# Performance work log

Hardware: AMD Instinct MI355X
Metric: run time of the kernel (lower is better)

Reference implementation:

```python
import jax, jax.numpy as jnp
import numpy as np

U, D, N, R = 256, 5120, 16, 160  # num_users, d_inner, d_state, dt_rank


def setup_inputs() -> dict:
    key = jax.random.key(0)
    ks = jax.random.split(key, 7)
    s = 0.02
    return {
        "x": jax.random.normal(ks[0], (U, D), jnp.float32),
        "delta_t_proj_w": jax.random.normal(ks[1], (D, R), jnp.float32) * s,
        "dt_proj_w": jax.random.normal(ks[2], (R, D), jnp.float32) * s,
        "dt_proj_b": jax.random.normal(ks[3], (D,), jnp.float32) * s,
        "B_proj_w": jax.random.normal(ks[4], (D, N), jnp.float32) * s,
        "abar": jax.random.uniform(ks[5], (U, D, N), jnp.float32),
        "hidden_state": jax.random.normal(ks[6], (U, D, N), jnp.float32),
    }


def reference(x, delta_t_proj_w, dt_proj_w, dt_proj_b, B_proj_w, abar, hidden_state):
    # delta: [U, D] -- low-rank dt projection then softplus
    dt = jax.nn.softplus(x @ delta_t_proj_w @ dt_proj_w + dt_proj_b)
    # B: [U, N]
    B = x @ B_proj_w
    # bbar[u,i,n] = dt[u,i] * B[u,n]  (discretized B, broadcast over d_inner x d_state)
    bbar = dt[:, :, None] * B[:, None, :]
    # h_new = abar * h + bbar * x   (selective-scan single step)
    h_new = abar * hidden_state + bbar * x[:, :, None]
    return h_new
```

## Files before the change

### kernel.cpp

```cpp
#include <hip/hip_runtime.h>
#include <math.h>

#define U_ 256
#define D_ 5120
#define N_ 16
#define R_ 160
#define J_ 176
#define KB 16

typedef float f4v __attribute__((ext_vector_type(4)));

__device__ __forceinline__ float softplus_f(float v) {
    return v > 20.f ? v : log1pf(__expf(v));
}

template<int NKS_T>
__global__ __launch_bounds__(256) void proj_partial(
    const float* __restrict__ x, const float* __restrict__ w1,
    const float* __restrict__ bw, float* __restrict__ P)
{
    constexpr int KSLAB_T = D_ / NKS_T;
    constexpr int STG_T   = KSLAB_T / KB;

    const int jt = blockIdx.x;
    const int ks = blockIdx.y;
    const int t  = threadIdx.x;
    const int uq = t & 63;
    const int jq = t >> 6;

    __shared__ float xs[KB][260];
    __shared__ float wsh[KB][16];

    const float* wptr; int ldw, jbase;
    if (jt < 10) { wptr = w1; ldw = R_; jbase = jt * 16; }
    else         { wptr = bw; ldw = N_; jbase = 0; }

    const int k0base = ks * KSLAB_T;
    const int ux = t >> 2;
    const int cx = t & 3;

    float acc[4][4] = {};

    float4 xr[4]; float4 wr = make_float4(0.f, 0.f, 0.f, 0.f);

    auto ld = [&](int s_, float4 (&xr_)[4], float4& wr_) {
        const int k0 = k0base + s_ * KB;
#pragma unroll
        for (int i = 0; i < 4; ++i)
            xr_[i] = *(const float4*)&x[(ux + i * 64) * D_ + k0 + cx * 4];
        if (t < 64) {
            const int k = t >> 2, c = t & 3;
            wr_ = *(const float4*)&wptr[(k0 + k) * ldw + jbase + c * 4];
        }
    };

    ld(0, xr, wr);

    for (int s = 0; s < STG_T; ++s) {
#pragma unroll
        for (int i = 0; i < 4; ++i) {
            const int u = ux + i * 64;
            xs[cx * 4 + 0][u] = xr[i].x;
            xs[cx * 4 + 1][u] = xr[i].y;
            xs[cx * 4 + 2][u] = xr[i].z;
            xs[cx * 4 + 3][u] = xr[i].w;
        }
        if (t < 64) *(float4*)&wsh[t >> 2][(t & 3) * 4] = wr;
        __syncthreads();

        float4 xr2[4]; float4 wr2 = make_float4(0.f, 0.f, 0.f, 0.f);
        if (s + 1 < STG_T) ld(s + 1, xr2, wr2);

#pragma unroll
        for (int kk = 0; kk < KB; ++kk) {
            const float4 wv = *(const float4*)&wsh[kk][jq * 4];
            const float4 av = *(const float4*)&xs[kk][uq * 4];
            const float avx[4] = {av.x, av.y, av.z, av.w};
            const float wvx[4] = {wv.x, wv.y, wv.z, wv.w};
#pragma unroll
            for (int i = 0; i < 4; ++i)
#pragma unroll
                for (int j = 0; j < 4; ++j)
                    acc[i][j] = fmaf(avx[i], wvx[j], acc[i][j]);
        }
        __syncthreads();
        if (s + 1 < STG_T) {
#pragma unroll
            for (int i = 0; i < 4; ++i) xr[i] = xr2[i];
            wr = wr2;
        }
    }

#pragma unroll
    for (int j = 0; j < 4; ++j) {
        float* row = P + ((size_t)ks * J_ + jt * 16 + jq * 4 + j) * 256;
        float4 v;
        v.x = acc[0][j]; v.y = acc[1][j]; v.z = acc[2][j]; v.w = acc[3][j];
        *(float4*)&row[uq * 4] = v;
    }
}

template<int NKS_T>
__global__ __launch_bounds__(256) void reduce_kernel(
    const float* __restrict__ P, float* __restrict__ tmpT,
    float* __restrict__ Bm)
{
    const int j = blockIdx.x;
    const int u = threadIdx.x;
    float sum = 0.f;
#pragma unroll 8
    for (int ks = 0; ks < NKS_T; ++ks)
        sum += P[((size_t)ks * J_ + j) * 256 + u];
    if (j < R_) tmpT[j * 256 + u] = sum;
    else        Bm[u * N_ + (j - R_)] = sum;
}

__global__ __launch_bounds__(64) void dt_kernel(
    const float* __restrict__ tmpT, const float* __restrict__ w2,
    const float* __restrict__ bias, const float* __restrict__ x,
    float* __restrict__ s)
{
    const int d0 = blockIdx.x * 64;
    const int u0 = blockIdx.y * 16;
    const int t  = threadIdx.x;
    const int du = t & 3;
    const int dd = t >> 4 == 0 ? (t >> 2) : (t >> 2);
    const int dq = t >> 2;

    __shared__ float ts[KB][16];
    __shared__ float ws_[KB][68];

    float acc[4][4] = {};

    const int rT = t >> 2, cT = t & 3;
    const int rw = t & 15, cw = t >> 4;

    for (int r0 = 0; r0 < R_; r0 += KB) {
        *(float4*)&ts[rT][cT * 4] =
            *(const float4*)&tmpT[(r0 + rT) * 256 + u0 + cT * 4];
#pragma unroll
        for (int q = 0; q < 4; ++q)
            *(float4*)&ws_[rw][(cw + q * 4) * 4] =
                *(const float4*)&w2[(r0 + rw) * D_ + d0 + (cw + q * 4) * 4];
        __syncthreads();
#pragma unroll
        for (int kk = 0; kk < KB; ++kk) {
            const float4 av = *(const float4*)&ts[kk][du * 4];
            const float4 wv = *(const float4*)&ws_[kk][dq * 4];
            const float avx[4] = {av.x, av.y, av.z, av.w};
            const float wvx[4] = {wv.x, wv.y, wv.z, wv.w};
#pragma unroll
            for (int i = 0; i < 4; ++i)
#pragma unroll
                for (int j = 0; j < 4; ++j)
                    acc[i][j] = fmaf(avx[i], wvx[j], acc[i][j]);
        }
        __syncthreads();
    }

    const int d = d0 + dq * 4;
    const float4 bv = *(const float4*)&bias[d];
#pragma unroll
    for (int i = 0; i < 4; ++i) {
        const int u = u0 + du * 4 + i;
        const float4 xv = *(const float4*)&x[u * D_ + d];
        float4 sv;
        sv.x = softplus_f(acc[i][0] + bv.x) * xv.x;
        sv.y = softplus_f(acc[i][1] + bv.y) * xv.y;
        sv.z = softplus_f(acc[i][2] + bv.z) * xv.z;
        sv.w = softplus_f(acc[i][3] + bv.w) * xv.w;
        *(float4*)&s[u * D_ + d] = sv;
    }
}

__global__ __launch_bounds__(256) void stream_kernel(
    const float* __restrict__ abar, const float* __restrict__ hs,
    const float* __restrict__ s, const float* __restrict__ Bm,
    float* __restrict__ out)
{
    const int u  = blockIdx.y;
    const int bx = blockIdx.x;
    const int t  = threadIdx.x;
    const float4* __restrict__ ab4 = (const float4*)abar;
    const float4* __restrict__ h4  = (const float4*)hs;
    f4v* o4 = (f4v*)out;

    const float* srow = s + u * D_;
    const float4 Bv = ((const float4*)Bm)[u * 4 + (t & 3)];
    const int base = u * (D_ * 4) + bx * 1024 + t;

    float4 av[4], hv[4];
    float  sv[4];
#pragma unroll
    for (int k = 0; k < 4; ++k) av[k] = ab4[base + k * 256];
#pragma unroll
    for (int k = 0; k < 4; ++k) hv[k] = h4[base + k * 256];
#pragma unroll
    for (int k = 0; k < 4; ++k) sv[k] = srow[(bx * 1024 + k * 256 + t) >> 2];
#pragma unroll
    for (int k = 0; k < 4; ++k) {
        f4v o;
        o.x = fmaf(av[k].x, hv[k].x, sv[k] * Bv.x);
        o.y = fmaf(av[k].y, hv[k].y, sv[k] * Bv.y);
        o.z = fmaf(av[k].z, hv[k].z, sv[k] * Bv.z);
        o.w = fmaf(av[k].w, hv[k].w, sv[k] * Bv.w);
        __builtin_nontemporal_store(o, &o4[base + k * 256]);
    }
}

extern "C" void kernel_launch(void* const* d_in, const int* in_sizes, int n_in,
                              void* d_out, int out_size, void* d_ws, size_t ws_size,
                              hipStream_t stream) {
    const float* x    = (const float*)d_in[0];
    const float* w1   = (const float*)d_in[1];
    const float* w2   = (const float*)d_in[2];
    const float* bias = (const float*)d_in[3];
    const float* bw   = (const float*)d_in[4];
    const float* abar = (const float*)d_in[5];
    const float* hs   = (const float*)d_in[6];
    float* out = (float*)d_out;

    float* P = (float*)d_ws;
    const size_t need64 = ((size_t)64 * J_ * 256 + (size_t)R_ * 256 +
                           (size_t)U_ * N_ + (size_t)U_ * D_) * sizeof(float);

    float *tmpT, *Bm, *s;
    if (ws_size >= need64) {
        tmpT = P + (size_t)64 * J_ * 256;
        Bm   = tmpT + R_ * 256;
        s    = Bm + U_ * N_;
        proj_partial<64><<<dim3(11, 64), 256, 0, stream>>>(x, w1, bw, P);
        reduce_kernel<64><<<dim3(J_), 256, 0, stream>>>(P, tmpT, Bm);
    } else {
        tmpT = P + (size_t)20 * J_ * 256;
        Bm   = tmpT + R_ * 256;
        s    = Bm + U_ * N_;
        proj_partial<20><<<dim3(11, 20), 256, 0, stream>>>(x, w1, bw, P);
        reduce_kernel<20><<<dim3(J_), 256, 0, stream>>>(P, tmpT, Bm);
    }
    dt_kernel<<<dim3(80, 16), 64, 0, stream>>>(tmpT, w2, bias, x, s);
    stream_kernel<<<dim3(20, 256), 256, 0, stream>>>(abar, hs, s, Bm, out);
}
```

Baseline: 261.0 us.

## Fuse all four stages into one cooperative persistent kernel with grid syncs

Replaces the four separate launches (projection partials, reduction, dt GEMM with softplus, streaming update) with a single cooperative kernel of 512 blocks that loops over tasks and separates phases with grid.sync. It also moves the K-split from 64 to 40 slabs, remaps the dt phase to 256-thread blocks, and uses nontemporal loads for abar and the hidden state. The aim is to remove launch gaps and tail effects between small kernels. In exchange it adds three grid-wide barriers and requires all 512 blocks to be co-resident. If the cooperative launch fails, it falls back to the old multi-kernel path.

```diff
diff --git a/kernel.cpp b/kernel.cpp
--- a/kernel.cpp
+++ b/kernel.cpp
@@ -1,5 +1,8 @@
 #include <hip/hip_runtime.h>
+#include <hip/hip_cooperative_groups.h>
 #include <math.h>
+
+namespace cg = cooperative_groups;
 
 #define U_ 256
 #define D_ 5120
@@ -7,11 +10,203 @@
 #define R_ 160
 #define J_ 176
 #define KB 16
+#define GRID_ 512
 
 typedef float f4v __attribute__((ext_vector_type(4)));
 
 __device__ __forceinline__ float softplus_f(float v) {
     return v > 20.f ? v : log1pf(__expf(v));
+}
+
+template<int NKS_T>
+__global__ __launch_bounds__(256, 2) void fused_all(
+    const float* __restrict__ x, const float* __restrict__ w1,
+    const float* __restrict__ w2, const float* __restrict__ bias,
+    const float* __restrict__ bw, const float* __restrict__ abar,
+    const float* __restrict__ hs, float* __restrict__ P,
+    float* __restrict__ tmpT, float* __restrict__ Bm,
+    float* __restrict__ s, float* __restrict__ out)
+{
+    constexpr int KSLAB_T = D_ / NKS_T;
+    constexpr int STG_T   = KSLAB_T / KB;
+
+    cg::grid_group grid = cg::this_grid();
+    const int bid = blockIdx.x;
+    const int t   = threadIdx.x;
+
+    __shared__ float xs[KB][260];
+    __shared__ float wsh[KB][16];
+    __shared__ float ts[KB][16];
+    __shared__ float ws2[KB][68];
+
+    {
+        const int uq = t & 63;
+        const int jq = t >> 6;
+        const int ux = t >> 2;
+        const int cx = t & 3;
+
+        for (int task = bid; task < 11 * NKS_T; task += GRID_) {
+            const int jt = task % 11;
+            const int ks = task / 11;
+
+            const float* wptr; int ldw, jbase;
+            if (jt < 10) { wptr = w1; ldw = R_; jbase = jt * 16; }
+            else         { wptr = bw; ldw = N_; jbase = 0; }
+
+            const int k0base = ks * KSLAB_T;
+
+            float acc[4][4] = {};
+            float4 xr[4]; float4 wr = make_float4(0.f, 0.f, 0.f, 0.f);
+
+            auto ld = [&](int s_, float4 (&xr_)[4], float4& wr_) {
+                const int k0 = k0base + s_ * KB;
+#pragma unroll
+                for (int i = 0; i < 4; ++i)
+                    xr_[i] = *(const float4*)&x[(ux + i * 64) * D_ + k0 + cx * 4];
+                if (t < 64) {
+                    const int k = t >> 2, c = t & 3;
+                    wr_ = *(const float4*)&wptr[(k0 + k) * ldw + jbase + c * 4];
+                }
+            };
+
+            ld(0, xr, wr);
+
+            for (int st = 0; st < STG_T; ++st) {
+#pragma unroll
+                for (int i = 0; i < 4; ++i) {
+                    const int u = ux + i * 64;
+                    xs[cx * 4 + 0][u] = xr[i].x;
+                    xs[cx * 4 + 1][u] = xr[i].y;
+                    xs[cx * 4 + 2][u] = xr[i].z;
+                    xs[cx * 4 + 3][u] = xr[i].w;
+                }
+                if (t < 64) *(float4*)&wsh[t >> 2][(t & 3) * 4] = wr;
+                __syncthreads();
+
+                float4 xr2[4]; float4 wr2 = make_float4(0.f, 0.f, 0.f, 0.f);
+                if (st + 1 < STG_T) ld(st + 1, xr2, wr2);
+
+#pragma unroll
+                for (int kk = 0; kk < KB; ++kk) {
+                    const float4 wv = *(const float4*)&wsh[kk][jq * 4];
+                    const float4 av = *(const float4*)&xs[kk][uq * 4];
+                    const float avx[4] = {av.x, av.y, av.z, av.w};
+                    const float wvx[4] = {wv.x, wv.y, wv.z, wv.w};
+#pragma unroll
+                    for (int i = 0; i < 4; ++i)
+#pragma unroll
+                        for (int j = 0; j < 4; ++j)
+                            acc[i][j] = fmaf(avx[i], wvx[j], acc[i][j]);
+                }
+                __syncthreads();
+                if (st + 1 < STG_T) {
+#pragma unroll
+                    for (int i = 0; i < 4; ++i) xr[i] = xr2[i];
+                    wr = wr2;
+                }
+            }
+
+#pragma unroll
+            for (int j = 0; j < 4; ++j) {
+                float* row = P + ((size_t)ks * J_ + jt * 16 + jq * 4 + j) * 256;
+                float4 v;
+                v.x = acc[0][j]; v.y = acc[1][j]; v.z = acc[2][j]; v.w = acc[3][j];
+                *(float4*)&row[uq * 4] = v;
+            }
+        }
+    }
+
+    grid.sync();
+
+    if (bid < J_) {
+        const int j = bid;
+        const int u = t;
+        float sum = 0.f;
+#pragma unroll 8
+        for (int ks = 0; ks < NKS_T; ++ks)
+            sum += P[((size_t)ks * J_ + j) * 256 + u];
+        if (j < R_) tmpT[j * 256 + u] = sum;
+        else        Bm[u * N_ + (j - R_)] = sum;
+    }
+
+    grid.sync();
+
+    {
+        const int uq = t >> 4;
+        const int dq = t & 15;
+        for (int task = bid; task < 80 * 16; task += GRID_) {
+            const int d0 = (task % 80) * 64;
+            const int u0 = (task / 80) * 16;
+
+            float acc[4] = {};
+
+            for (int r0 = 0; r0 < R_; r0 += KB) {
+                if (t < 64)
+                    *(float4*)&ts[t >> 2][(t & 3) * 4] =
+                        *(const float4*)&tmpT[(r0 + (t >> 2)) * 256 + u0 + (t & 3) * 4];
+                *(float4*)&ws2[t >> 4][(t & 15) * 4] =
+                    *(const float4*)&w2[(r0 + (t >> 4)) * D_ + d0 + (t & 15) * 4];
+                __syncthreads();
+#pragma unroll
+                for (int kk = 0; kk < KB; ++kk) {
+                    const float  a  = ts[kk][uq];
+                    const float4 wv = *(const float4*)&ws2[kk][dq * 4];
+                    acc[0] = fmaf(a, wv.x, acc[0]);
+                    acc[1] = fmaf(a, wv.y, acc[1]);
+                    acc[2] = fmaf(a, wv.z, acc[2]);
+                    acc[3] = fmaf(a, wv.w, acc[3]);
+                }
+                __syncthreads();
+            }
+
+            const int d = d0 + dq * 4;
+            const int u = u0 + uq;
+            const float4 bv = *(const float4*)&bias[d];
+            const float4 xv = *(const float4*)&x[u * D_ + d];
+            float4 sv;
+            sv.x = softplus_f(acc[0] + bv.x) * xv.x;
+            sv.y = softplus_f(acc[1] + bv.y) * xv.y;
+            sv.z = softplus_f(acc[2] + bv.z) * xv.z;
+            sv.w = softplus_f(acc[3] + bv.w) * xv.w;
+            *(float4*)&s[u * D_ + d] = sv;
+        }
+    }
+
+    grid.sync();
+
+    {
+        const int u        = bid >> 1;
+        const int halfbase = (bid & 1) * 10240;
+        const f4v* __restrict__ ab4 = (const f4v*)abar;
+        const f4v* __restrict__ h4  = (const f4v*)hs;
+        f4v* o4 = (f4v*)out;
+
+        const float* srow = s + u * D_;
+        const f4v Bv = ((const f4v*)Bm)[u * 4 + (t & 3)];
+        const size_t ub = (size_t)u * 20480 + halfbase;
+
+        for (int i = 0; i < 40; i += 4) {
+            f4v av[4], hv[4]; float sv[4];
+#pragma unroll
+            for (int k = 0; k < 4; ++k)
+                av[k] = __builtin_nontemporal_load(&ab4[ub + (size_t)(i + k) * 256 + t]);
+#pragma unroll
+            for (int k = 0; k < 4; ++k)
+                hv[k] = __builtin_nontemporal_load(&h4[ub + (size_t)(i + k) * 256 + t]);
+#pragma unroll
+            for (int k = 0; k < 4; ++k)
+                sv[k] = srow[(halfbase + (i + k) * 256 + t) >> 2];
+#pragma unroll
+            for (int k = 0; k < 4; ++k) {
+                f4v o;
+                o.x = fmaf(av[k].x, hv[k].x, sv[k] * Bv.x);
+                o.y = fmaf(av[k].y, hv[k].y, sv[k] * Bv.y);
+                o.z = fmaf(av[k].z, hv[k].z, sv[k] * Bv.z);
+                o.w = fmaf(av[k].w, hv[k].w, sv[k] * Bv.w);
+                __builtin_nontemporal_store(o, &o4[ub + (size_t)(i + k) * 256 + t]);
+            }
+        }
+    }
 }
 
 template<int NKS_T>
@@ -40,7 +235,6 @@
     const int cx = t & 3;
 
     float acc[4][4] = {};
-
     float4 xr[4]; float4 wr = make_float4(0.f, 0.f, 0.f, 0.f);
 
     auto ld = [&](int s_, float4 (&xr_)[4], float4& wr_) {
@@ -56,7 +250,7 @@
 
     ld(0, xr, wr);
 
-    for (int s = 0; s < STG_T; ++s) {
+    for (int st = 0; st < STG_T; ++st) {
 #pragma unroll
         for (int i = 0; i < 4; ++i) {
             const int u = ux + i * 64;
@@ -69,7 +263,7 @@
         __syncthreads();
 
         float4 xr2[4]; float4 wr2 = make_float4(0.f, 0.f, 0.f, 0.f);
-        if (s + 1 < STG_T) ld(s + 1, xr2, wr2);
+        if (st + 1 < STG_T) ld(st + 1, xr2, wr2);
 
 #pragma unroll
         for (int kk = 0; kk < KB; ++kk) {
@@ -84,7 +278,7 @@
                     acc[i][j] = fmaf(avx[i], wvx[j], acc[i][j]);
         }
         __syncthreads();
-        if (s + 1 < STG_T) {
+        if (st + 1 < STG_T) {
 #pragma unroll
             for (int i = 0; i < 4; ++i) xr[i] = xr2[i];
             wr = wr2;
@@ -124,7 +318,6 @@
     const int u0 = blockIdx.y * 16;
     const int t  = threadIdx.x;
     const int du = t & 3;
-    const int dd = t >> 4 == 0 ? (t >> 2) : (t >> 2);
     const int dq = t >> 2;
 
     __shared__ float ts[KB][16];
@@ -221,23 +414,40 @@
     float* out = (float*)d_out;
 
     float* P = (float*)d_ws;
-    const size_t need64 = ((size_t)64 * J_ * 256 + (size_t)R_ * 256 +
+
+    const size_t need40 = ((size_t)40 * J_ * 256 + (size_t)R_ * 256 +
                            (size_t)U_ * N_ + (size_t)U_ * D_) * sizeof(float);
 
+    hipError_t err;
     float *tmpT, *Bm, *s;
-    if (ws_size >= need64) {
-        tmpT = P + (size_t)64 * J_ * 256;
+
+    if (ws_size >= need40) {
+        tmpT = P + (size_t)40 * J_ * 256;
         Bm   = tmpT + R_ * 256;
         s    = Bm + U_ * N_;
-        proj_partial<64><<<dim3(11, 64), 256, 0, stream>>>(x, w1, bw, P);
-        reduce_kernel<64><<<dim3(J_), 256, 0, stream>>>(P, tmpT, Bm);
+        void* args[] = { (void*)&x, (void*)&w1, (void*)&w2, (void*)&bias,
+                         (void*)&bw, (void*)&abar, (void*)&hs, (void*)&P,
+                         (void*)&tmpT, (void*)&Bm, (void*)&s, (void*)&out };
+        err = hipLaunchCooperativeKernel((const void*)(&fused_all<40>),
+                                         dim3(GRID_), dim3(256), args, 0, stream);
     } else {
+        tmpT = P + (size_t)20 * J_ * 256;
+        Bm   = tmpT + R_ * 256;
+        s    = Bm + U_ * N_;
+        void* args[] = { (void*)&x, (void*)&w1, (void*)&w2, (void*)&bias,
+                         (void*)&bw, (void*)&abar, (void*)&hs, (void*)&P,
+                         (void*)&tmpT, (void*)&Bm, (void*)&s, (void*)&out };
+        err = hipLaunchCooperativeKernel((const void*)(&fused_all<20>),
+                                         dim3(GRID_), dim3(256), args, 0, stream);
+    }
+
+    if (err != hipSuccess) {
         tmpT = P + (size_t)20 * J_ * 256;
         Bm   = tmpT + R_ * 256;
         s    = Bm + U_ * N_;
         proj_partial<20><<<dim3(11, 20), 256, 0, stream>>>(x, w1, bw, P);
         reduce_kernel<20><<<dim3(J_), 256, 0, stream>>>(P, tmpT, Bm);
-    }
-    dt_kernel<<<dim3(80, 16), 64, 0, stream>>>(tmpT, w2, bias, x, s);
-    stream_kernel<<<dim3(20, 256), 256, 0, stream>>>(abar, hs, s, Bm, out);
-}
+        dt_kernel<<<dim3(80, 16), 64, 0, stream>>>(tmpT, w2, bias, x, s);
+        stream_kernel<<<dim3(20, 256), 256, 0, stream>>>(abar, hs, s, Bm, out);
+    }
+}
```

Result: slower. 449.8 us (+72.3%).
